# Kernel optimization log

Hardware: AMD Instinct MI355X
Metric: run time of the kernel (lower is better)

## Reference

```python
import jax, jax.numpy as jnp
from jax import lax
import numpy as np

DIM = 384
NUM_HEADS = 8
HEAD_DIM = DIM // NUM_HEADS


def setup_inputs() -> dict:
    key = jax.random.key(0)
    k_x, k_qw, k_qb, k_lw, k_lb = jax.random.split(key, 5)
    B, H, W = 2, 64, 64
    N = H * W
    x = jax.random.normal(k_x, (B, N, DIM), dtype=jnp.float32)
    # nn.Linear(dim, 3*dim): weight (3C, C), bias (3C,)
    qkv_w = jax.random.normal(k_qw, (3 * DIM, DIM), dtype=jnp.float32) * (1.0 / np.sqrt(DIM))
    qkv_b = jax.random.normal(k_qb, (3 * DIM,), dtype=jnp.float32) * 0.02
    # nn.Conv2d(dim, dim, 3, padding=1, groups=dim): weight (C, 1, 3, 3), bias (C,)
    lepe_w = jax.random.normal(k_lw, (DIM, 1, 3, 3), dtype=jnp.float32) * (1.0 / 3.0)
    lepe_b = jax.random.normal(k_lb, (DIM,), dtype=jnp.float32) * 0.02
    return {"x": x, "qkv_w": qkv_w, "qkv_b": qkv_b, "lepe_w": lepe_w, "lepe_b": lepe_b, "H": H, "W": W}


def reference(x, qkv_w, qkv_b, lepe_w, lepe_b, H, W):
    B, N, C = x.shape
    hd = C // NUM_HEADS
    scale = hd ** -0.5
    # qkv projection: (B, N, 3C) -> (B, N, 3, heads, head_dim)
    qkv = (jnp.einsum('bnc,oc->bno', x, qkv_w) + qkv_b).reshape(B, N, 3, NUM_HEADS, hd)
    q, k, v = qkv[:, :, 0], qkv[:, :, 1], qkv[:, :, 2]  # each (B, N, heads, hd)
    attn = jnp.einsum('bnhd,bmhd->bhnm', q * scale, k)   # (B, heads, N, N)
    attn = jax.nn.softmax(attn, axis=-1)
    out = jnp.einsum('bhnm,bmhd->bnhd', attn, v).reshape(B, N, C)
    # LePE: depthwise 3x3 conv on v in NCHW layout
    v_img = v.reshape(B, H, W, C).transpose(0, 3, 1, 2)  # (B, C, H, W)
    lepe = lax.conv_general_dilated(
        v_img, lepe_w, window_strides=(1, 1), padding='SAME',
        feature_group_count=C,
        dimension_numbers=('NCHW', 'OIHW', 'NCHW'))
    lepe = lepe + lepe_b[None, :, None, None]
    return out + lepe.transpose(0, 2, 3, 1).reshape(B, N, C)
```

## Files before the change

kernel.cpp:

```cpp
#include <hip/hip_runtime.h>
#include <stdint.h>

#define DIM   384
#define NH    8
#define HD    48
#define NTOK  4096
#define KDIM  384
#define SCALEL2E 0.20823509610f

typedef float  f32x4   __attribute__((ext_vector_type(4)));
typedef float  f32x16  __attribute__((ext_vector_type(16)));
typedef __bf16 bf16x8  __attribute__((ext_vector_type(8)));

#if __has_builtin(__builtin_amdgcn_exp2f)
#define EXP2F(x) __builtin_amdgcn_exp2f(x)
#else
#define EXP2F(x) exp2f(x)
#endif

__device__ __forceinline__ unsigned short f2bf(float f) {
  union { float f; unsigned int u; } c; c.f = f;
  unsigned int r = (c.u + 0x7FFFu + ((c.u >> 16) & 1u)) >> 16;
  return (unsigned short)r;
}
__device__ __forceinline__ float bf2f(unsigned short h) {
  union { unsigned int u; float f; } c; c.u = ((unsigned int)h) << 16;
  return c.f;
}


__global__ void prep_kernel(const float* __restrict__ x, const float* __restrict__ w,
                            unsigned short* __restrict__ x_bf,
                            unsigned short* __restrict__ w_bf) {
  int tid = blockIdx.x * blockDim.x + threadIdx.x;
  int stride = gridDim.x * blockDim.x;
  for (int i = tid; i < 786432; i += stride) {
    float4 v = ((const float4*)x)[i];
    ushort4 o;
    o.x = f2bf(v.x); o.y = f2bf(v.y); o.z = f2bf(v.z); o.w = f2bf(v.w);
    ((ushort4*)x_bf)[i] = o;
  }
  for (int i = tid; i < 110592; i += stride) {
    float4 v = ((const float4*)w)[i];
    ushort4 o;
    o.x = f2bf(v.x); o.y = f2bf(v.y); o.z = f2bf(v.z); o.w = f2bf(v.w);
    ((ushort4*)w_bf)[i] = o;
  }
}

__global__ __launch_bounds__(256) void qkv_gemm(
    const unsigned short* __restrict__ A,
    const unsigned short* __restrict__ Bw,
    const float* __restrict__ bias,
    unsigned short* __restrict__ qc,
    unsigned short* __restrict__ kc,
    unsigned short* __restrict__ v_t) {
  __shared__ unsigned short ldsA[128 * 32];
  __shared__ unsigned short ldsB[64 * 32];
  const int tid = threadIdx.x;
  const int wv = tid >> 6, ln = tid & 63;
  const int lrow = ln & 15, lq = ln >> 4;
  const int m0 = blockIdx.x * 128;
  const int n0 = blockIdx.y * 64;
  const int wm = (wv >> 1) * 64, wn = (wv & 1) * 32;

  f32x4 acc[4][2];
#pragma unroll
  for (int mi = 0; mi < 4; ++mi)
#pragma unroll
    for (int ni = 0; ni < 2; ++ni)
#pragma unroll
      for (int r = 0; r < 4; ++r) acc[mi][ni][r] = 0.f;

  for (int k0 = 0; k0 < KDIM; k0 += 32) {
    __syncthreads();
#pragma unroll
    for (int j = 0; j < 2; ++j) {
      int r16 = wv * 2 + j;
      const unsigned short* ga = A + (size_t)(m0 + r16 * 16 + (ln >> 2)) * KDIM
                                   + k0 + (ln & 3) * 8;
      __builtin_amdgcn_global_load_lds(
          (const __attribute__((address_space(1))) void*)ga,
          (__attribute__((address_space(3))) void*)&ldsA[r16 * 512], 16, 0, 0);
    }
    const unsigned short* gb = Bw + (size_t)(n0 + wv * 16 + (ln >> 2)) * KDIM
                                  + k0 + (ln & 3) * 8;
    __builtin_amdgcn_global_load_lds(
        (const __attribute__((address_space(1))) void*)gb,
        (__attribute__((address_space(3))) void*)&ldsB[wv * 512], 16, 0, 0);
    __syncthreads();
    bf16x8 af[4], bfv[2];
#pragma unroll
    for (int mi = 0; mi < 4; ++mi)
      af[mi] = *(const bf16x8*)&ldsA[(wm + mi * 16 + lrow) * 32 + lq * 8];
#pragma unroll
    for (int ni = 0; ni < 2; ++ni)
      bfv[ni] = *(const bf16x8*)&ldsB[(wn + ni * 16 + lrow) * 32 + lq * 8];
#pragma unroll
    for (int mi = 0; mi < 4; ++mi)
#pragma unroll
      for (int ni = 0; ni < 2; ++ni)
        acc[mi][ni] = __builtin_amdgcn_mfma_f32_16x16x32_bf16(
            af[mi], bfv[ni], acc[mi][ni], 0, 0, 0);
  }

#pragma unroll
  for (int mi = 0; mi < 4; ++mi)
#pragma unroll
    for (int ni = 0; ni < 2; ++ni)
#pragma unroll
      for (int r = 0; r < 4; ++r) {
        int row = m0 + wm + mi * 16 + lq * 4 + r;
        int col = n0 + wn + ni * 16 + lrow;
        float val = acc[mi][ni][r] + bias[col];
        int b = row >> 12;
        int n = row & 4095;
        if (col < 384) {
          int h = col / 48, d = col - h * 48;
          qc[((size_t)(b * 8 + h) * NTOK + n) * HD + d] = f2bf(val * SCALEL2E);
        } else if (col < 768) {
          int o = col - 384;
          int h = o / 48, d = o - h * 48;
          kc[((size_t)(b * 8 + h) * NTOK + n) * HD + d] = f2bf(val);
        } else {
          int o = col - 768;
          v_t[((size_t)b * DIM + o) * NTOK + n] = f2bf(val);
        }
      }
}

__global__ __launch_bounds__(256) void lepe_kernel(
    const unsigned short* __restrict__ v_t,
    const float* __restrict__ lw, const float* __restrict__ lb,
    float* __restrict__ out) {
  __shared__ __align__(16) unsigned short pl[16 * 648];
  const int cg = blockIdx.x;
  const int sy = blockIdx.y;
  const int b  = blockIdx.z;
  const int t = threadIdx.x;
  const int y0 = sy * 8;
#pragma unroll
  for (int i = 0; i < 5; ++i) {
    int id = t + i * 256;
    int c = id / 80, rem = id - c * 80;
    int row = rem >> 3, cx = rem & 7;
    int y = y0 - 1 + row;
    uint4 val = make_uint4(0u, 0u, 0u, 0u);
    if (y >= 0 && y < 64)
      val = *(const uint4*)(v_t + ((size_t)(b * DIM + cg * 16 + c)) * NTOK + y * 64 + cx * 8);
    *(uint4*)&pl[c * 648 + row * 64 + cx * 8] = val;
  }
  __syncthreads();
  const int c = t & 15, pg = t >> 4;
  const int cglob = cg * 16 + c;
  float w[9];
#pragma unroll
  for (int j = 0; j < 9; ++j) w[j] = lw[cglob * 9 + j];
  const float bias = lb[cglob];
  const unsigned short* base = &pl[c * 648];
  for (int i = 0; i < 32; ++i) {
    int p = pg * 32 + i;
    int lr = p >> 6, x = p & 63;
    float acc = bias;
#pragma unroll
    for (int ky = 0; ky < 3; ++ky)
#pragma unroll
      for (int kx = 0; kx < 3; ++kx) {
        int xx = x + kx - 1;
        if (xx >= 0 && xx < 64)
          acc += w[ky * 3 + kx] * bf2f(base[(lr + ky) * 64 + xx]);
      }
    out[((size_t)(b * NTOK + sy * 512 + p)) * DIM + cglob] = acc;
  }
}

__global__ __launch_bounds__(256, 4) void attn_kernel(
    const unsigned short* __restrict__ qc,
    const unsigned short* __restrict__ kcg,
    const unsigned short* __restrict__ v_t,
    float* __restrict__ out) {
  __shared__ __align__(16) char smem[31232];
  unsigned short* Kl = (unsigned short*)smem;
  unsigned short* Vl = (unsigned short*)(smem + 14336);
  float* Lsum = (float*)(smem + 30720);
  float* Ol   = (float*)smem;

  const int tid = threadIdx.x;
  const int wv = tid >> 6, ln = tid & 63;
  const int kh = wv >> 1;
  const int wq = wv & 1;
  const int l31 = ln & 31, hh = ln >> 5;
  const int th = tid & 127;
  const int qb = blockIdx.x, bh = blockIdx.y;
  const int b = bh >> 3, hd = bh & 7;

  unsigned short* Kh = Kl + kh * 3584;
  unsigned short* Vh = Vl + kh * 4096;

  int kro[3], kgo[3], vro[3], vgo[3];
#pragma unroll
  for (int i = 0; i < 3; ++i) {
    int idx = th + i * 128;
    int r = idx / 6, cc = idx - r * 6;
    kro[i] = r * 56 + cc * 8;
    kgo[i] = r * 48 + cc * 8;
    int vd = idx >> 3, vc = idx & 7;
    vro[i] = vd * 64 + ((vc ^ (vd & 7)) * 8);
    vgo[i] = vd * 4096 + vc * 8;
  }

  if (th < 8) {
    uint4 one4 = make_uint4(0x3F803F80u, 0x3F803F80u, 0x3F803F80u, 0x3F803F80u);
    *(uint4*)&Vh[3072 + th * 8] = one4;
  }

  const int qrb_self = wq * 32 + l31;
  const unsigned short* qp = qc + ((size_t)bh * NTOK + qb * 64 + qrb_self) * HD + hh * 8;
  bf16x8 Qf[3];
#pragma unroll
  for (int hs = 0; hs < 3; ++hs)
    Qf[hs] = *(const bf16x8*)(qp + hs * 16);

  f32x16 Oacc[2];
#pragma unroll
  for (int dc = 0; dc < 2; ++dc)
#pragma unroll
    for (int r = 0; r < 16; ++r) Oacc[dc][r] = 0.f;

  const unsigned short* kbase = kcg + (size_t)bh * NTOK * HD;
  const unsigned short* vbase = v_t + ((size_t)b * DIM + hd * HD) * NTOK;

  for (int it = 0; it < 32; ++it) {
    const int kt = kh * 32 + it;
    __syncthreads();
    const unsigned short* kg = kbase + (size_t)kt * 64 * HD;
    const unsigned short* vg = vbase + kt * 64;
#pragma unroll
    for (int i = 0; i < 3; ++i) {
      *(uint4*)&Kh[kro[i]] = *(const uint4*)(kg + kgo[i]);
      *(uint4*)&Vh[vro[i]] = *(const uint4*)(vg + vgo[i]);
    }
    __syncthreads();

    unsigned int P32[16];
#pragma unroll
    for (int C = 0; C < 2; ++C) {
      f32x16 s;
#pragma unroll
      for (int r = 0; r < 16; ++r) s[r] = 0.f;
      const unsigned short* kr = &Kh[(C * 32 + l31) * 56 + hh * 8];
#pragma unroll
      for (int hs = 0; hs < 3; ++hs) {
        bf16x8 kf = *(const bf16x8*)(kr + hs * 16);
        s = __builtin_amdgcn_mfma_f32_32x32x16_bf16(kf, Qf[hs], s, 0, 0, 0);
      }
#pragma unroll
      for (int t8 = 0; t8 < 8; ++t8) {
        float e0 = EXP2F(s[2 * t8]);
        float e1 = EXP2F(s[2 * t8 + 1]);
        P32[C * 8 + t8] = __builtin_amdgcn_perm(
            __float_as_uint(e1), __float_as_uint(e0), 0x07060302u);
      }
    }

#pragma unroll
    for (int s4 = 0; s4 < 4; ++s4) {
      const int o = (s4 >> 1) * 8 + (s4 & 1) * 4;
      unsigned int send1 = hh ? P32[o + 0] : P32[o + 2];
      unsigned int send2 = hh ? P32[o + 1] : P32[o + 3];
      unsigned int recv1 = (unsigned int)__shfl_xor((int)send1, 32, 64);
      unsigned int recv2 = (unsigned int)__shfl_xor((int)send2, 32, 64);
      union { unsigned int u[4]; bf16x8 v; } pa;
      pa.u[0] = hh ? recv1 : P32[o + 0];
      pa.u[1] = hh ? recv2 : P32[o + 1];
      pa.u[2] = hh ? P32[o + 2] : recv1;
      pa.u[3] = hh ? P32[o + 3] : recv2;
#pragma unroll
      for (int dc = 0; dc < 2; ++dc) {
        int vrow = dc * 32 + l31;
        bf16x8 vf = *(const bf16x8*)&Vh[vrow * 64 + (((s4 * 2 + hh) ^ (vrow & 7)) * 8)];
        Oacc[dc] = __builtin_amdgcn_mfma_f32_32x32x16_bf16(pa.v, vf, Oacc[dc], 0, 0, 0);
      }
    }
  }

  __syncthreads();
  if (l31 == 16) {
#pragma unroll
    for (int r = 0; r < 16; ++r) {
      int qrb = wq * 32 + (r & 3) + 8 * (r >> 2) + 4 * hh;
      Lsum[kh * 64 + qrb] = Oacc[1][r];
    }
  }
  if (kh == 1) {
#pragma unroll
    for (int r = 0; r < 16; ++r) {
      int qrb = wq * 32 + (r & 3) + 8 * (r >> 2) + 4 * hh;
      Ol[qrb * 48 + l31] = Oacc[0][r];
      if (l31 < 16) Ol[qrb * 48 + 32 + l31] = Oacc[1][r];
    }
  }
  __syncthreads();
  if (kh == 0) {
#pragma unroll
    for (int r = 0; r < 16; ++r) {
      int qrb = wq * 32 + (r & 3) + 8 * (r >> 2) + 4 * hh;
      float linv = 1.0f / (Lsum[qrb] + Lsum[64 + qrb]);
      float* op = out + ((size_t)(b * NTOK + qb * 64 + qrb)) * DIM + hd * HD;
      op[l31] += (Oacc[0][r] + Ol[qrb * 48 + l31]) * linv;
      if (l31 < 16) op[32 + l31] += (Oacc[1][r] + Ol[qrb * 48 + 32 + l31]) * linv;
    }
  }
}

extern "C" void kernel_launch(void* const* d_in, const int* in_sizes, int n_in,
                              void* d_out, int out_size, void* d_ws, size_t ws_size,
                              hipStream_t stream) {
  const float* x      = (const float*)d_in[0];
  const float* qkv_w  = (const float*)d_in[1];
  const float* qkv_b  = (const float*)d_in[2];
  const float* lepe_w = (const float*)d_in[3];
  const float* lepe_b = (const float*)d_in[4];

  char* ws = (char*)d_ws;
  unsigned short* x_bf = (unsigned short*)(ws);
  unsigned short* w_bf = (unsigned short*)(ws + 6291456);
  unsigned short* qcp  = (unsigned short*)(ws + 7176192);
  unsigned short* kcp  = (unsigned short*)(ws + 13467648);
  unsigned short* v_t  = (unsigned short*)(ws + 19759104);
  float* out = (float*)d_out;

  prep_kernel<<<1024, 256, 0, stream>>>(x, qkv_w, x_bf, w_bf);
  qkv_gemm<<<dim3(64, 18), 256, 0, stream>>>(x_bf, w_bf, qkv_b, qcp, kcp, v_t);
  lepe_kernel<<<dim3(24, 8, 2), 256, 0, stream>>>(v_t, lepe_w, lepe_b, out);
  attn_kernel<<<dim3(64, 16), 256, 0, stream>>>(qcp, kcp, v_t, out);
}
```

Baseline: 198.4 us.

## Fuse LePE conv into attention epilogue, stage GEMM stores via LDS, swizzle K

Removes the separate LePE kernel and computes the depthwise 3x3 conv for each query row tile inside the attention kernel's epilogue, writing the output once instead of doing a read-modify-write. The QKV GEMM epilogue now stages results through shared memory so it can issue 16-byte coalesced stores, including a transposed store for V. The K tile in LDS changes from padded rows to an XOR-swizzled layout with a 64-element stride. The costs are more LDS per attention block, which may lower occupancy, and uncoalesced global reads of V for the conv inside the attention kernel.

```diff
diff --git a/kernel.cpp b/kernel.cpp
--- a/kernel.cpp
+++ b/kernel.cpp
@@ -57,6 +57,7 @@
     unsigned short* __restrict__ v_t) {
   __shared__ unsigned short ldsA[128 * 32];
   __shared__ unsigned short ldsB[64 * 32];
+  __shared__ unsigned short ebuf[64 * 72];
   const int tid = threadIdx.x;
   const int wv = tid >> 6, ln = tid & 63;
   const int lrow = ln & 15, lq = ln >> 4;
@@ -104,73 +105,58 @@
             af[mi], bfv[ni], acc[mi][ni], 0, 0, 0);
   }
 
-#pragma unroll
-  for (int mi = 0; mi < 4; ++mi)
-#pragma unroll
-    for (int ni = 0; ni < 2; ++ni)
-#pragma unroll
-      for (int r = 0; r < 4; ++r) {
-        int row = m0 + wm + mi * 16 + lq * 4 + r;
-        int col = n0 + wn + ni * 16 + lrow;
-        float val = acc[mi][ni][r] + bias[col];
-        int b = row >> 12;
-        int n = row & 4095;
-        if (col < 384) {
-          int h = col / 48, d = col - h * 48;
-          qc[((size_t)(b * 8 + h) * NTOK + n) * HD + d] = f2bf(val * SCALEL2E);
-        } else if (col < 768) {
-          int o = col - 384;
-          int h = o / 48, d = o - h * 48;
-          kc[((size_t)(b * 8 + h) * NTOK + n) * HD + d] = f2bf(val);
-        } else {
-          int o = col - 768;
-          v_t[((size_t)b * DIM + o) * NTOK + n] = f2bf(val);
-        }
-      }
-}
-
-__global__ __launch_bounds__(256) void lepe_kernel(
-    const unsigned short* __restrict__ v_t,
-    const float* __restrict__ lw, const float* __restrict__ lb,
-    float* __restrict__ out) {
-  __shared__ __align__(16) unsigned short pl[16 * 648];
-  const int cg = blockIdx.x;
-  const int sy = blockIdx.y;
-  const int b  = blockIdx.z;
-  const int t = threadIdx.x;
-  const int y0 = sy * 8;
-#pragma unroll
-  for (int i = 0; i < 5; ++i) {
-    int id = t + i * 256;
-    int c = id / 80, rem = id - c * 80;
-    int row = rem >> 3, cx = rem & 7;
-    int y = y0 - 1 + row;
-    uint4 val = make_uint4(0u, 0u, 0u, 0u);
-    if (y >= 0 && y < 64)
-      val = *(const uint4*)(v_t + ((size_t)(b * DIM + cg * 16 + c)) * NTOK + y * 64 + cx * 8);
-    *(uint4*)&pl[c * 648 + row * 64 + cx * 8] = val;
-  }
-  __syncthreads();
-  const int c = t & 15, pg = t >> 4;
-  const int cglob = cg * 16 + c;
-  float w[9];
-#pragma unroll
-  for (int j = 0; j < 9; ++j) w[j] = lw[cglob * 9 + j];
-  const float bias = lb[cglob];
-  const unsigned short* base = &pl[c * 648];
-  for (int i = 0; i < 32; ++i) {
-    int p = pg * 32 + i;
-    int lr = p >> 6, x = p & 63;
-    float acc = bias;
-#pragma unroll
-    for (int ky = 0; ky < 3; ++ky)
-#pragma unroll
-      for (int kx = 0; kx < 3; ++kx) {
-        int xx = x + kx - 1;
-        if (xx >= 0 && xx < 64)
-          acc += w[ky * 3 + kx] * bf2f(base[(lr + ky) * 64 + xx]);
-      }
-    out[((size_t)(b * NTOK + sy * 512 + p)) * DIM + cglob] = acc;
+  const int region = (n0 >= 768) ? 2 : (n0 >= 384 ? 1 : 0);
+  const float scl = (region == 0) ? SCALEL2E : 1.0f;
+  const float bias0 = bias[n0 + wn + lrow];
+  const float bias1 = bias[n0 + wn + 16 + lrow];
+
+#pragma unroll
+  for (int half = 0; half < 2; ++half) {
+    __syncthreads();
+    if ((wv >> 1) == half) {
+#pragma unroll
+      for (int mi = 0; mi < 4; ++mi)
+#pragma unroll
+        for (int ni = 0; ni < 2; ++ni)
+#pragma unroll
+          for (int r = 0; r < 4; ++r) {
+            int row = mi * 16 + lq * 4 + r;
+            int col = wn + ni * 16 + lrow;
+            float val = (acc[mi][ni][r] + (ni ? bias1 : bias0)) * scl;
+            ebuf[row * 72 + col] = f2bf(val);
+          }
+    }
+    __syncthreads();
+    if (region < 2) {
+      unsigned short* dst = (region == 0) ? qc : kc;
+      const int obase = n0 - region * 384;
+#pragma unroll
+      for (int i = 0; i < 2; ++i) {
+        int id = tid + i * 256;
+        int row = id >> 3, cc = id & 7;
+        uint4 val = *(const uint4*)&ebuf[row * 72 + cc * 8];
+        int nrow = m0 + half * 64 + row;
+        int b = nrow >> 12, nn = nrow & 4095;
+        int o = obase + cc * 8;
+        int h = o / 48, d = o - h * 48;
+        *(uint4*)&dst[((size_t)(b * 8 + h) * NTOK + nn) * HD + d] = val;
+      }
+    } else {
+#pragma unroll
+      for (int i = 0; i < 2; ++i) {
+        int id = tid + i * 256;
+        int col = id & 63, rc = id >> 6;
+        int r0 = rc * 8;
+        union { unsigned short s[8]; uint4 u; } pk;
+#pragma unroll
+        for (int j = 0; j < 8; ++j)
+          pk.s[j] = ebuf[(r0 + j) * 72 + col];
+        int nrow = m0 + half * 64 + r0;
+        int b = nrow >> 12;
+        int o = n0 - 768 + col;
+        *(uint4*)&v_t[((size_t)(b * DIM + o)) * NTOK + (nrow & 4095)] = pk.u;
+      }
+    }
   }
 }
 
@@ -178,11 +164,12 @@
     const unsigned short* __restrict__ qc,
     const unsigned short* __restrict__ kcg,
     const unsigned short* __restrict__ v_t,
+    const float* __restrict__ lw, const float* __restrict__ lb,
     float* __restrict__ out) {
-  __shared__ __align__(16) char smem[31232];
+  __shared__ __align__(16) char smem[33280];
   unsigned short* Kl = (unsigned short*)smem;
-  unsigned short* Vl = (unsigned short*)(smem + 14336);
-  float* Lsum = (float*)(smem + 30720);
+  unsigned short* Vl = (unsigned short*)(smem + 16384);
+  float* Lsum = (float*)(smem + 32768);
   float* Ol   = (float*)smem;
 
   const int tid = threadIdx.x;
@@ -194,7 +181,7 @@
   const int qb = blockIdx.x, bh = blockIdx.y;
   const int b = bh >> 3, hd = bh & 7;
 
-  unsigned short* Kh = Kl + kh * 3584;
+  unsigned short* Kh = Kl + kh * 4096;
   unsigned short* Vh = Vl + kh * 4096;
 
   int kro[3], kgo[3], vro[3], vgo[3];
@@ -202,7 +189,7 @@
   for (int i = 0; i < 3; ++i) {
     int idx = th + i * 128;
     int r = idx / 6, cc = idx - r * 6;
-    kro[i] = r * 56 + cc * 8;
+    kro[i] = r * 64 + ((cc ^ (r & 7)) * 8);
     kgo[i] = r * 48 + cc * 8;
     int vd = idx >> 3, vc = idx & 7;
     vro[i] = vd * 64 + ((vc ^ (vd & 7)) * 8);
@@ -248,10 +235,12 @@
       f32x16 s;
 #pragma unroll
       for (int r = 0; r < 16; ++r) s[r] = 0.f;
-      const unsigned short* kr = &Kh[(C * 32 + l31) * 56 + hh * 8];
+      const int krow = C * 32 + l31;
+      const unsigned short* kr = &Kh[krow * 64];
+      const int rx = krow & 7;
 #pragma unroll
       for (int hs = 0; hs < 3; ++hs) {
-        bf16x8 kf = *(const bf16x8*)(kr + hs * 16);
+        bf16x8 kf = *(const bf16x8*)&kr[((hs * 2 + hh) ^ rx) * 8];
         s = __builtin_amdgcn_mfma_f32_32x32x16_bf16(kf, Qf[hs], s, 0, 0, 0);
       }
 #pragma unroll
@@ -292,12 +281,37 @@
       Lsum[kh * 64 + qrb] = Oacc[1][r];
     }
   }
+  {
+    const int px = tid & 63;
+    const int c0 = (tid >> 6) * 12;
+    const int y = qb;
+    const unsigned short* vpl = v_t + ((size_t)b * DIM + hd * HD) * NTOK;
+    for (int cj = 0; cj < 12; ++cj) {
+      int c = c0 + cj;
+      const float* wp = lw + (size_t)(hd * HD + c) * 9;
+      float a = lb[hd * HD + c];
+      const unsigned short* pl = vpl + (size_t)c * NTOK + y * 64 + px;
+#pragma unroll
+      for (int dy = -1; dy <= 1; ++dy) {
+        if ((unsigned)(y + dy) < 64u) {
+#pragma unroll
+          for (int dx = -1; dx <= 1; ++dx) {
+            if ((unsigned)(px + dx) < 64u)
+              a += wp[(dy + 1) * 3 + (dx + 1)] * bf2f(pl[dy * 64 + dx]);
+          }
+        }
+      }
+      Ol[px * 48 + c] = a;
+    }
+  }
+  __syncthreads();
   if (kh == 1) {
 #pragma unroll
     for (int r = 0; r < 16; ++r) {
       int qrb = wq * 32 + (r & 3) + 8 * (r >> 2) + 4 * hh;
-      Ol[qrb * 48 + l31] = Oacc[0][r];
-      if (l31 < 16) Ol[qrb * 48 + 32 + l31] = Oacc[1][r];
+      float linv = 1.0f / (Lsum[qrb] + Lsum[64 + qrb]);
+      Ol[qrb * 48 + l31] += Oacc[0][r] * linv;
+      if (l31 < 16) Ol[qrb * 48 + 32 + l31] += Oacc[1][r] * linv;
     }
   }
   __syncthreads();
@@ -307,8 +321,8 @@
       int qrb = wq * 32 + (r & 3) + 8 * (r >> 2) + 4 * hh;
       float linv = 1.0f / (Lsum[qrb] + Lsum[64 + qrb]);
       float* op = out + ((size_t)(b * NTOK + qb * 64 + qrb)) * DIM + hd * HD;
-      op[l31] += (Oacc[0][r] + Ol[qrb * 48 + l31]) * linv;
-      if (l31 < 16) op[32 + l31] += (Oacc[1][r] + Ol[qrb * 48 + 32 + l31]) * linv;
+      op[l31] = Ol[qrb * 48 + l31] + Oacc[0][r] * linv;
+      if (l31 < 16) op[32 + l31] = Ol[qrb * 48 + 32 + l31] + Oacc[1][r] * linv;
     }
   }
 }
@@ -332,6 +346,5 @@
 
   prep_kernel<<<1024, 256, 0, stream>>>(x, qkv_w, x_bf, w_bf);
   qkv_gemm<<<dim3(64, 18), 256, 0, stream>>>(x_bf, w_bf, qkv_b, qcp, kcp, v_t);
-  lepe_kernel<<<dim3(24, 8, 2), 256, 0, stream>>>(v_t, lepe_w, lepe_b, out);
-  attn_kernel<<<dim3(64, 16), 256, 0, stream>>>(qcp, kcp, v_t, out);
-}
+  attn_kernel<<<dim3(64, 16), 256, 0, stream>>>(qcp, kcp, v_t, lepe_w, lepe_b, out);
+}
```

After: 213.4 us. +7.6%, slower.
